# Kernel optimization log

Measured on AMD Instinct MI355X. Metric: run time of the kernel, lower is better.

## Reference

```python
import jax, jax.numpy as jnp
import numpy as np

K_INTERACT = 8  # k nearest context nodes per target hyperedge


def setup_inputs() -> dict:
    key = jax.random.key(0)
    ks = jax.random.split(key, 7)
    B, C, H, W = 4, 256, 64, 64
    s = 1.0 / np.sqrt(C).astype(np.float32)
    return {
        "X_target": jax.random.normal(ks[0], (B, C, H, W), jnp.float32),
        "X_context1": jax.random.normal(ks[1], (B, C, H, W), jnp.float32),
        "X_context2": jax.random.normal(ks[2], (B, C, H, W), jnp.float32),
        # HypergraphConv params: node2edge Linear (W1,b1), edge2node Linear (W2,b2)
        "W1": jax.random.normal(ks[3], (C, C), jnp.float32) * s,
        "b1": jax.random.normal(ks[4], (C,), jnp.float32) * s,
        "W2": jax.random.normal(ks[5], (C, C), jnp.float32) * s,
        "b2": jax.random.normal(ks[6], (C,), jnp.float32) * s,
    }


def _hypergraph_one(Xt, Xc, W1, b1, W2, b2, k):
    """Per-batch hypergraph message passing, sparse form of H^T X / H X.
    Xt: [N, C] target nodes, Xc: [Nc, C] context nodes.
    Edge j = {target j} U {k nearest context nodes of target j}.
    Equivalent to dense H_i [N+Nc, N] with degree normalization.
    """
    N, C = Xt.shape
    Nc = Xc.shape[0]
    # squared Euclidean cdist (same argmins as torch.cdist), knn = smallest-k
    d2 = (jnp.sum(Xt * Xt, axis=1)[:, None]
          + jnp.sum(Xc * Xc, axis=1)[None, :]
          - 2.0 * (Xt @ Xc.T))                      # [N, Nc]
    _, knn = jax.lax.top_k(-d2, k)                   # [N, k] context indices

    # node2edge linear transform on all nodes
    Xn_t = Xt @ W1 + b1                              # [N, C]
    Xn_c = Xc @ W1 + b1                              # [Nc, C]

    # X_edge = (H^T @ Xn) / deg_e ; deg_e = k+1 (self + k distinct knn)
    gathered = Xn_c[knn]                             # [N, k, C]
    X_edge = (Xn_t + gathered.sum(axis=1)) / jnp.float32(k + 1)

    # edge2node linear transform
    X_et = X_edge @ W2 + b2                          # [N, C]

    # X_node_new = (H @ X_et) / deg_v
    # target node v belongs only to edge v -> deg_v = 1
    out_t = X_et
    # context node c sums X_et[j] over edges j that selected it
    flat = knn.reshape(-1)                           # [N*k]
    contrib = jax.ops.segment_sum(
        jnp.broadcast_to(X_et[:, None, :], (N, k, C)).reshape(N * k, C),
        flat, num_segments=Nc)                       # [Nc, C]
    counts = jax.ops.segment_sum(jnp.ones((N * k,), jnp.float32),
                                 flat, num_segments=Nc)
    out_c = contrib / jnp.clip(counts, 1.0)[:, None]  # deg_v clamp_min(1)
    return out_t, out_c


def reference(X_target, X_context1, X_context2, W1, b1, W2, b2):
    B, C, H, W = X_target.shape
    N = H * W
    to_nodes = lambda x: x.transpose(0, 2, 3, 1).reshape(B, N, C)
    Xt = to_nodes(X_target)                                       # [B, N, C]
    Xc = jnp.concatenate([to_nodes(X_context1), to_nodes(X_context2)],
                         axis=1)                                  # [B, 2N, C]
    f = lambda xt, xc: _hypergraph_one(xt, xc, W1, b1, W2, b2, K_INTERACT)
    out_t, out_c = jax.vmap(f)(Xt, Xc)
    to_img = lambda x: x.reshape(B, H, W, C).transpose(0, 3, 1, 2)
    return (to_img(out_t), to_img(out_c[:, :N]), to_img(out_c[:, N:]))
```

## Files before the change

kernel.cpp:

```cpp
#include <hip/hip_runtime.h>
#include <math.h>
#include <float.h>

#define BATCH 4
#define CH    256
#define NT    4096
#define NCTX  8192
#define KI    8

#define CSEL    10
#define DNSPLIT 8
#define CTX_PER (NCTX / DNSPLIT)
#define NTILE   (CTX_PER / 32)
#define NKEY    (DNSPLIT * CSEL)
#define RESC    12

typedef __attribute__((ext_vector_type(8)))  __bf16 bf16x8;
typedef __attribute__((ext_vector_type(16))) float  f32x16;

__device__ __forceinline__ unsigned short bf16_rne(float v) {
  unsigned u = __float_as_uint(v);
  return (unsigned short)((u + 0x7fffu + ((u >> 16) & 1u)) >> 16);
}

__global__ __launch_bounds__(256) void k_transpose2(const float* __restrict__ Xt,
                                                    const float* __restrict__ Xc1,
                                                    const float* __restrict__ Xc2,
                                                    float* __restrict__ Q,
                                                    float* __restrict__ P,
                                                    unsigned short* __restrict__ XtBh,
                                                    unsigned short* __restrict__ XtBl,
                                                    unsigned short* __restrict__ XcBh,
                                                    unsigned short* __restrict__ XcBl,
                                                    float* __restrict__ nrm) {
  __shared__ float tile[64][33];
  __shared__ float ps[8][32];
  const int which = blockIdx.z >> 2, b = blockIdx.z & 3;
  const float* src;
  float* dF; unsigned short *dH, *dL; float* nrmp = nullptr;
  if (which == 0) {
    src = Xt + (long)b * CH * NT;
    dF = Q + (long)b * NT * CH;
    dH = XtBh + (long)b * NT * CH;  dL = XtBl + (long)b * NT * CH;
  } else if (which == 1) {
    src = Xc1 + (long)b * CH * NT;
    dF = P + (long)b * NCTX * CH;
    dH = XcBh + (long)b * NCTX * CH;  dL = XcBl + (long)b * NCTX * CH;
    nrmp = nrm + (long)b * NCTX;
  } else {
    src = Xc2 + (long)b * CH * NT;
    dF = P + ((long)b * NCTX + NT) * CH;
    dH = XcBh + ((long)b * NCTX + NT) * CH;  dL = XcBl + ((long)b * NCTX + NT) * CH;
    nrmp = nrm + (long)b * NCTX + NT;
  }
  const int m0 = blockIdx.x * 32, c0 = blockIdx.y * 64;
  const int tx = threadIdx.x, ty = threadIdx.y;
  float part = 0.f;
#pragma unroll
  for (int i = ty; i < 64; i += 8) {
    float v = src[(long)(c0 + i) * NT + (m0 + tx)];
    tile[i][tx] = v;
    part = fmaf(v, v, part);
  }
  if (which) ps[ty][tx] = part;
  __syncthreads();
#pragma unroll
  for (int i = ty; i < 32; i += 8) {
    float v0 = tile[2 * tx][i];
    float v1 = tile[2 * tx + 1][i];
    long o = (long)(m0 + i) * CH + (c0 + 2 * tx);
    float2 f2; f2.x = v0; f2.y = v1;
    *(float2*)&dF[o] = f2;
    unsigned short h0 = bf16_rne(v0), h1 = bf16_rne(v1);
    ushort2 h2; h2.x = h0; h2.y = h1;
    *(ushort2*)&dH[o] = h2;
    float hf0 = __uint_as_float((unsigned)h0 << 16);
    float hf1 = __uint_as_float((unsigned)h1 << 16);
    ushort2 l2; l2.x = bf16_rne(v0 - hf0); l2.y = bf16_rne(v1 - hf1);
    *(ushort2*)&dL[o] = l2;
  }
  if (which && ty == 0) {
    float s = 0.f;
#pragma unroll
    for (int j = 0; j < 8; ++j) s += ps[j][tx];
    atomicAdd(&nrmp[m0 + tx], -0.5f * s);
  }
}

__global__ __launch_bounds__(256) void k_wtrans(const float* __restrict__ W1,
                                                const float* __restrict__ W2,
                                                unsigned short* __restrict__ WT1h,
                                                unsigned short* __restrict__ WT1l,
                                                unsigned short* __restrict__ WT2h,
                                                unsigned short* __restrict__ WT2l) {
  __shared__ float tile[32][33];
  const float* W = blockIdx.z ? W2 : W1;
  unsigned short* WTh = blockIdx.z ? WT2h : WT1h;
  unsigned short* WTl = blockIdx.z ? WT2l : WT1l;
  const int n0 = blockIdx.x * 32, k0 = blockIdx.y * 32;
  const int tx = threadIdx.x, ty = threadIdx.y;
#pragma unroll
  for (int i = ty; i < 32; i += 8)
    tile[i][tx] = W[(k0 + i) * CH + (n0 + tx)];
  __syncthreads();
#pragma unroll
  for (int i = ty; i < 32; i += 8) {
    float v = tile[tx][i];
    int o = (n0 + i) * CH + (k0 + tx);
    unsigned short h = bf16_rne(v);
    WTh[o] = h;
    float hf = __uint_as_float((unsigned)h << 16);
    WTl[o] = bf16_rne(v - hf);
  }
}

__global__ __launch_bounds__(256) void k_dist_mfma(const __bf16* __restrict__ XcB,
                                                   const __bf16* __restrict__ XtB,
                                                   const float* __restrict__ nrm,
                                                   unsigned* __restrict__ cand) {
  __shared__ __bf16 lds[2][32 * CH];
  const int lid = blockIdx.x;
  const int xk = lid & 7;
  const int b = xk >> 1, jh = xk & 1;
  const int jw = (lid >> 3) & 15, split = lid >> 7;
  const int t = threadIdx.x, w = t >> 6, lane = t & 63;
  const int l31 = lane & 31, lh = lane >> 5;
  const int tgt0 = (jh * 16 + jw) * 128 + w * 32;
  const int cbase = split * CTX_PER;
  const float* nrmt = nrm + (long)b * NCTX + cbase;

  const __bf16* tp = XtB + ((long)b * NT + tgt0 + l31) * CH + lh * 8;
  bf16x8 bfrag[16];
#pragma unroll
  for (int s = 0; s < 16; ++s) bfrag[s] = *(const bf16x8*)(tp + s * 16);

  unsigned kd[CSEL];
#pragma unroll
  for (int q = 0; q < CSEL; ++q) kd[q] = 0xFFFFFFFFu;

  const __bf16* cp = XcB + ((long)b * NCTX + cbase + l31) * CH;

  auto STAGE = [&](int buf, int jt) {
#pragma unroll
    for (int r = 0; r < 4; ++r) {
      int c = r * 4 + w;
      const __bf16* src = cp + (long)jt * 32 * CH + (c * 2 + lh) * 8;
      __bf16* dst = &lds[buf][c * 512];
      __builtin_amdgcn_global_load_lds((const __attribute__((address_space(1))) void*)src,
                                       (__attribute__((address_space(3))) void*)dst,
                                       16, 0, 0);
    }
  };

  STAGE(0, 0);
  __syncthreads();

  int cur = 0;
  for (int jt = 0; jt < NTILE; ++jt) {
    if (jt + 1 < NTILE) STAGE(cur ^ 1, jt + 1);

    const int ct0 = jt * 32;
    f32x16 acc;
#pragma unroll
    for (int g = 0; g < 4; ++g) {
      float4 nv = *(const float4*)&nrmt[ct0 + 8 * g + 4 * lh];
      acc[4 * g + 0] = nv.x; acc[4 * g + 1] = nv.y;
      acc[4 * g + 2] = nv.z; acc[4 * g + 3] = nv.w;
    }
#pragma unroll
    for (int s = 0; s < 16; ++s) {
      bf16x8 a = *(const bf16x8*)(&lds[cur][s * 512 + lane * 8]);
      acc = __builtin_amdgcn_mfma_f32_32x32x16_bf16(a, bfrag[s], acc, 0, 0, 0);
    }

#pragma unroll
    for (int reg = 0; reg < 16; ++reg) {
      const int row = (reg & 3) + 8 * (reg >> 2) + lh * 4;
      float sc = fmaf(acc[reg], -2.0f, 512.0f);
      unsigned key = (__float_as_uint(sc) & 0xFFFFF800u) | (unsigned)ct0 | (unsigned)row;
#pragma unroll
      for (int q = 0; q < CSEL; ++q) {
        unsigned lo = min(key, kd[q]);
        key = max(key, kd[q]);
        kd[q] = lo;
      }
    }
    __syncthreads();
    cur ^= 1;
  }

  unsigned oth[CSEL];
#pragma unroll
  for (int q = 0; q < CSEL; ++q) oth[q] = (unsigned)__shfl_xor((int)kd[q], 32, 64);
  if (lh == 0) {
    long ob = (((long)b * NT + tgt0 + l31) * DNSPLIT + split) * CSEL;
#pragma unroll
    for (int q = 0; q < CSEL; ++q)
      cand[ob + q] = min(kd[q], oth[CSEL - 1 - q]);
  }
}

__global__ __launch_bounds__(64) void k_rescore(const float* __restrict__ XtT,
                                                const float* __restrict__ XcT,
                                                const unsigned* __restrict__ cand,
                                                int* __restrict__ knn,
                                                unsigned* __restrict__ counts) {
  const int n = blockIdx.x, b = blockIdx.y, lane = threadIdx.x;
  const int grp = lane >> 4, gl = lane & 15;
  __shared__ unsigned sk[NKEY];
  __shared__ int cidx[RESC];
  __shared__ double sd[RESC];
  __shared__ int sj[RESC];
  const unsigned* kp = cand + ((long)b * NT + n) * NKEY;
  unsigned k0 = kp[lane];
  unsigned k1 = (lane < NKEY - 64) ? kp[64 + lane] : 0xFFFFFFFFu;
  sk[lane] = k0;
  if (lane < NKEY - 64) sk[64 + lane] = k1;
  __syncthreads();
  int r0 = 0, r1 = 0;
  for (int i = 0; i < NKEY; ++i) {
    unsigned s = sk[i];
    r0 += (s < k0 || (s == k0 && i < lane)) ? 1 : 0;
    r1 += (s < k1 || (s == k1 && i < 64 + lane)) ? 1 : 0;
  }
  if (r0 < RESC) cidx[r0] = (lane / CSEL) * CTX_PER + (int)(k0 & 0x7FFu);
  if (lane < NKEY - 64 && r1 < RESC)
    cidx[r1] = ((64 + lane) / CSEL) * CTX_PER + (int)(k1 & 0x7FFu);
  __syncthreads();

  const float* xt = XtT + ((long)b * NT + n) * CH + gl * 16;
  double xa[16];
#pragma unroll
  for (int r = 0; r < 4; ++r) {
    float4 v = *(const float4*)(xt + r * 4);
    xa[4 * r + 0] = (double)v.x; xa[4 * r + 1] = (double)v.y;
    xa[4 * r + 2] = (double)v.z; xa[4 * r + 3] = (double)v.w;
  }
#pragma unroll
  for (int q0 = 0; q0 < RESC; q0 += 4) {
    int q = q0 + grp;
    int j = cidx[q];
    const float* xc = XcT + ((long)b * NCTX + j) * CH + gl * 16;
    double acc = 0.0;
#pragma unroll
    for (int r = 0; r < 4; ++r) {
      float4 v = *(const float4*)(xc + r * 4);
      double d0 = xa[4 * r + 0] - (double)v.x; acc = fma(d0, d0, acc);
      double d1 = xa[4 * r + 1] - (double)v.y; acc = fma(d1, d1, acc);
      double d2 = xa[4 * r + 2] - (double)v.z; acc = fma(d2, d2, acc);
      double d3 = xa[4 * r + 3] - (double)v.w; acc = fma(d3, d3, acc);
    }
#pragma unroll
    for (int off = 8; off > 0; off >>= 1) acc += __shfl_xor(acc, off, 64);
    if (gl == 0) { sd[q] = acc; sj[q] = j; }
  }
  __syncthreads();
  double dq = (lane < RESC) ? sd[lane] : DBL_MAX;
  int    jq = (lane < RESC) ? sj[lane] : 0x7fffffff;
  int rank = 0;
#pragma unroll
  for (int i = 0; i < RESC; ++i) {
    double di = sd[i]; int ji = sj[i];
    rank += (di < dq || (di == dq && ji < jq)) ? 1 : 0;
  }
  if (lane < RESC && rank < KI) {
    knn[((long)b * NT + n) * KI + rank] = jq;
    atomicAdd(&counts[(long)b * NCTX + jq], 1u);
  }
}

__global__ __launch_bounds__(256) void k_gemm_mfma(const unsigned short* __restrict__ Ah,
                                                   const unsigned short* __restrict__ Al,
                                                   const unsigned short* __restrict__ WTh,
                                                   const unsigned short* __restrict__ WTl,
                                                   const float* __restrict__ bias,
                                                   float* __restrict__ out, int M) {
  __shared__ __bf16 ldsH[32 * CH];
  __shared__ __bf16 ldsL[32 * CH];
  const int b = blockIdx.y;
  const int m0 = blockIdx.x * 32;
  const int t = threadIdx.x, w = t >> 6, lane = t & 63;
  const int l31 = lane & 31, lh = lane >> 5;
  const long abase = (long)b * M * CH;
  const unsigned short* pH = Ah + abase + (long)(m0 + l31) * CH;
  const unsigned short* pL = Al + abase + (long)(m0 + l31) * CH;
#pragma unroll
  for (int r = 0; r < 4; ++r) {
    int c = r * 4 + w;
    __builtin_amdgcn_global_load_lds(
        (const __attribute__((address_space(1))) void*)(pH + (c * 2 + lh) * 8),
        (__attribute__((address_space(3))) void*)&ldsH[c * 512], 16, 0, 0);
    __builtin_amdgcn_global_load_lds(
        (const __attribute__((address_space(1))) void*)(pL + (c * 2 + lh) * 8),
        (__attribute__((address_space(3))) void*)&ldsL[c * 512], 16, 0, 0);
  }
  __syncthreads();

  const int n0 = w * 64;
  f32x16 acc0, acc1;
#pragma unroll
  for (int i = 0; i < 16; ++i) { acc0[i] = 0.f; acc1[i] = 0.f; }
#pragma unroll
  for (int s = 0; s < 16; ++s) {
    bf16x8 ah = *(const bf16x8*)&ldsH[s * 512 + lane * 8];
    bf16x8 al = *(const bf16x8*)&ldsL[s * 512 + lane * 8];
    const int koff = lh * 8 + s * 16;
    bf16x8 bh0 = *(const bf16x8*)&WTh[(n0 + l31) * CH + koff];
    bf16x8 bl0 = *(const bf16x8*)&WTl[(n0 + l31) * CH + koff];
    bf16x8 bh1 = *(const bf16x8*)&WTh[(n0 + 32 + l31) * CH + koff];
    bf16x8 bl1 = *(const bf16x8*)&WTl[(n0 + 32 + l31) * CH + koff];
    acc0 = __builtin_amdgcn_mfma_f32_32x32x16_bf16(ah, bh0, acc0, 0, 0, 0);
    acc1 = __builtin_amdgcn_mfma_f32_32x32x16_bf16(ah, bh1, acc1, 0, 0, 0);
    acc0 = __builtin_amdgcn_mfma_f32_32x32x16_bf16(ah, bl0, acc0, 0, 0, 0);
    acc1 = __builtin_amdgcn_mfma_f32_32x32x16_bf16(ah, bl1, acc1, 0, 0, 0);
    acc0 = __builtin_amdgcn_mfma_f32_32x32x16_bf16(al, bh0, acc0, 0, 0, 0);
    acc1 = __builtin_amdgcn_mfma_f32_32x32x16_bf16(al, bh1, acc1, 0, 0, 0);
  }
  float* ob = out + abase;
  float bi0 = bias[n0 + l31], bi1 = bias[n0 + 32 + l31];
#pragma unroll
  for (int reg = 0; reg < 16; ++reg) {
    int row = (reg & 3) + 8 * (reg >> 2) + 4 * lh;
    ob[(long)(m0 + row) * CH + n0 + l31]      = acc0[reg] + bi0;
    ob[(long)(m0 + row) * CH + n0 + 32 + l31] = acc1[reg] + bi1;
  }
}

__global__ __launch_bounds__(256) void k_gather(const float* __restrict__ Xn_t,
                                                const float* __restrict__ Xn_c,
                                                const int* __restrict__ knn,
                                                unsigned short* __restrict__ XeH,
                                                unsigned short* __restrict__ XeL) {
  const int n = blockIdx.x, b = blockIdx.y, c = threadIdx.x;
  const int* kn = knn + ((long)b * NT + n) * KI;
  int j[KI];
#pragma unroll
  for (int q = 0; q < KI; ++q) j[q] = kn[q];
  float acc = Xn_t[((long)b * NT + n) * CH + c];
#pragma unroll
  for (int q = 0; q < KI; ++q) acc += Xn_c[((long)b * NCTX + j[q]) * CH + c];
  float xe = acc / 9.0f;
  long o = ((long)b * NT + n) * CH + c;
  unsigned short h = bf16_rne(xe);
  XeH[o] = h;
  float hf = __uint_as_float((unsigned)h << 16);
  XeL[o] = bf16_rne(xe - hf);
}

__global__ __launch_bounds__(256) void k_g2f(const unsigned short* __restrict__ XeH_g,
                                             const unsigned short* __restrict__ XeL_g,
                                             const unsigned short* __restrict__ WTh,
                                             const unsigned short* __restrict__ WTl,
                                             const float* __restrict__ bias,
                                             float* __restrict__ out_t,
                                             float* __restrict__ R) {
  __shared__ char smem[34816];
  __bf16* ldsH = (__bf16*)smem;
  __bf16* ldsL = (__bf16*)(smem + 16384);
  const int b = blockIdx.y;
  const int m0 = blockIdx.x * 32;
  const int t = threadIdx.x, w = t >> 6, lane = t & 63;
  const int l31 = lane & 31, lh = lane >> 5;
  const long abase = (long)b * NT * CH;
  const unsigned short* pH = XeH_g + abase + (long)(m0 + l31) * CH;
  const unsigned short* pL = XeL_g + abase + (long)(m0 + l31) * CH;
#pragma unroll
  for (int r = 0; r < 4; ++r) {
    int c = r * 4 + w;
    __builtin_amdgcn_global_load_lds(
        (const __attribute__((address_space(1))) void*)(pH + (c * 2 + lh) * 8),
        (__attribute__((address_space(3))) void*)&ldsH[c * 512], 16, 0, 0);
    __builtin_amdgcn_global_load_lds(
        (const __attribute__((address_space(1))) void*)(pL + (c * 2 + lh) * 8),
        (__attribute__((address_space(3))) void*)&ldsL[c * 512], 16, 0, 0);
  }
  __syncthreads();

  const unsigned short* wh0 = WTh + (long)(w * 64 + l31) * CH;
  const unsigned short* wl0 = WTl + (long)(w * 64 + l31) * CH;
  f32x16 acc0, acc1;
#pragma unroll
  for (int i = 0; i < 16; ++i) { acc0[i] = 0.f; acc1[i] = 0.f; }
#pragma unroll
  for (int s = 0; s < 16; ++s) {
    const int koff = lh * 8 + s * 16;
    bf16x8 beh = *(const bf16x8*)&ldsH[s * 512 + lane * 8];
    bf16x8 bel = *(const bf16x8*)&ldsL[s * 512 + lane * 8];
    bf16x8 ah0 = *(const bf16x8*)(const __bf16*)(wh0 + koff);
    bf16x8 al0 = *(const bf16x8*)(const __bf16*)(wl0 + koff);
    bf16x8 ah1 = *(const bf16x8*)(const __bf16*)(wh0 + 32 * CH + koff);
    bf16x8 al1 = *(const bf16x8*)(const __bf16*)(wl0 + 32 * CH + koff);
    acc0 = __builtin_amdgcn_mfma_f32_32x32x16_bf16(ah0, beh, acc0, 0, 0, 0);
    acc1 = __builtin_amdgcn_mfma_f32_32x32x16_bf16(ah1, beh, acc1, 0, 0, 0);
    acc0 = __builtin_amdgcn_mfma_f32_32x32x16_bf16(al0, beh, acc0, 0, 0, 0);
    acc1 = __builtin_amdgcn_mfma_f32_32x32x16_bf16(al1, beh, acc1, 0, 0, 0);
    acc0 = __builtin_amdgcn_mfma_f32_32x32x16_bf16(ah0, bel, acc0, 0, 0, 0);
    acc1 = __builtin_amdgcn_mfma_f32_32x32x16_bf16(ah1, bel, acc1, 0, 0, 0);
  }
  __syncthreads();

  float* S = (float*)smem;
  float* ot = out_t + (long)b * CH * NT + m0;
#pragma unroll
  for (int reg = 0; reg < 16; ++reg) {
    const int row = (reg & 3) + 8 * (reg >> 2) + 4 * lh;
    const int ch0 = w * 64 + row, ch1 = ch0 + 32;
    float v0 = acc0[reg] + bias[ch0];
    float v1 = acc1[reg] + bias[ch1];
    S[ch0 * 33 + l31] = v0;
    S[ch1 * 33 + l31] = v1;
    ot[(long)ch0 * NT + l31] = v0;
    ot[(long)ch1 * NT + l31] = v1;
  }
  __syncthreads();
  const int n = t & 31, cg = t >> 5;
  float* rrow = R + ((long)b * NT + m0 + n) * CH;
#pragma unroll
  for (int kk = 0; kk < 8; ++kk) {
    const int c = cg * 32 + kk * 4;
    float4 v;
    v.x = S[(c + 0) * 33 + n];
    v.y = S[(c + 1) * 33 + n];
    v.z = S[(c + 2) * 33 + n];
    v.w = S[(c + 3) * 33 + n];
    *(float4*)(rrow + c) = v;
  }
}

__global__ __launch_bounds__(256) void k_scatter(const float* __restrict__ Xet,
                                                 const int* __restrict__ knn,
                                                 float* __restrict__ contrib) {
  const int n = blockIdx.x, b = blockIdx.y, c = threadIdx.x;
  const float v = Xet[((long)b * NT + n) * CH + c];
  const int* kn = knn + ((long)b * NT + n) * KI;
#pragma unroll
  for (int q = 0; q < KI; ++q)
    atomicAdd(&contrib[((long)b * NCTX + kn[q]) * CH + c], v);
}

__global__ __launch_bounds__(256) void k_fin_c(const float* __restrict__ contrib,
                                               const unsigned* __restrict__ counts,
                                               float* __restrict__ out1,
                                               float* __restrict__ out2) {
  __shared__ float tile[32][33];
  const int b = blockIdx.z;
  const int j0 = blockIdx.x * 32, c0 = blockIdx.y * 32;
  const int tx = threadIdx.x, ty = threadIdx.y;
#pragma unroll
  for (int i = ty; i < 32; i += 8) {
    float cnt = fmaxf((float)counts[(long)b * NCTX + j0 + i], 1.0f);
    tile[i][tx] = contrib[((long)b * NCTX + j0 + i) * CH + c0 + tx] / cnt;
  }
  __syncthreads();
  float* outp = (j0 < NT) ? (out1 + (long)b * CH * NT + j0)
                          : (out2 + (long)b * CH * NT + (j0 - NT));
#pragma unroll
  for (int i = ty; i < 32; i += 8)
    outp[(long)(c0 + i) * NT + tx] = tile[tx][i];
}

extern "C" void kernel_launch(void* const* d_in, const int* in_sizes, int n_in,
                              void* d_out, int out_size, void* d_ws, size_t ws_size,
                              hipStream_t stream) {
  const float* Xt  = (const float*)d_in[0];
  const float* Xc1 = (const float*)d_in[1];
  const float* Xc2 = (const float*)d_in[2];
  const float* W1  = (const float*)d_in[3];
  const float* b1  = (const float*)d_in[4];
  const float* W2  = (const float*)d_in[5];
  const float* b2  = (const float*)d_in[6];
  float* out = (float*)d_out;

  float* P = (float*)d_ws;
  float* Q = P + (long)BATCH * NCTX * CH;
  float* R = Q + (long)BATCH * NT * CH;
  float* nrm = R + (long)BATCH * NT * CH;
  unsigned* counts = (unsigned*)(nrm + (long)BATCH * NCTX);
  int* knn = (int*)(counts + (long)BATCH * NCTX);
  unsigned short* WT1h = (unsigned short*)(knn + (long)BATCH * NT * KI);
  unsigned short* WT1l = WT1h + CH * CH;
  unsigned short* WT2h = WT1l + CH * CH;
  unsigned short* WT2l = WT2h + CH * CH;

  unsigned* cand = (unsigned*)R;

  unsigned short* XcBh = (unsigned short*)d_out;
  unsigned short* XtBh = XcBh + (long)BATCH * NCTX * CH;
  unsigned short* XcBl = XtBh + (long)BATCH * NT * CH;
  unsigned short* XtBl = XcBl + (long)BATCH * NCTX * CH;

  float* Xn_c = P;
  float* Xn_t = R;
  unsigned short* XeH = (unsigned short*)Q;
  unsigned short* XeL = XeH + (long)BATCH * NT * CH;

  float* out_t  = out;
  float* out_c1 = out + (long)BATCH * CH * NT;
  float* out_c2 = out + 2L * BATCH * CH * NT;

  dim3 tb(32, 8);

  hipMemsetAsync(nrm, 0, (size_t)BATCH * NCTX * 8, stream);

  k_wtrans<<<dim3(8, 8, 2), tb, 0, stream>>>(W1, W2, WT1h, WT1l, WT2h, WT2l);

  k_transpose2<<<dim3(NT / 32, CH / 64, 12), tb, 0, stream>>>(
      Xt, Xc1, Xc2, Q, P, XtBh, XtBl, XcBh, XcBl, nrm);

  k_dist_mfma<<<dim3(8 * 16 * DNSPLIT), 256, 0, stream>>>(
      (const __bf16*)XcBh, (const __bf16*)XtBh, nrm, cand);

  k_rescore<<<dim3(NT, BATCH), 64, 0, stream>>>(Q, P, cand, knn, counts);

  k_gemm_mfma<<<dim3(NT / 32, BATCH), 256, 0, stream>>>(XtBh, XtBl, WT1h, WT1l, b1, Xn_t, NT);
  k_gemm_mfma<<<dim3(NCTX / 32, BATCH), 256, 0, stream>>>(XcBh, XcBl, WT1h, WT1l, b1, Xn_c, NCTX);

  k_gather<<<dim3(NT, BATCH), 256, 0, stream>>>(Xn_t, Xn_c, knn, XeH, XeL);

  hipMemsetAsync(P, 0, (size_t)BATCH * NCTX * CH * 4, stream);

  k_g2f<<<dim3(NT / 32, BATCH), 256, 0, stream>>>(XeH, XeL, WT2h, WT2l, b2, out_t, R);

  k_scatter<<<dim3(NT, BATCH), 256, 0, stream>>>(R, knn, P);
  k_fin_c<<<dim3(NCTX / 32, CH / 32, BATCH), tb, 0, stream>>>(P, counts, out_c1, out_c2);
}
```

Measured before the change: 437.1 us.

## Merge distance kNN and node2edge GEMMs into one launch; fuse prep kernels

The weight transpose is merged into the input transpose/split kernel, which also widens its tiles to 128 channels and writes float4/ushort4 vectors. When the workspace is large enough, the distance top-k kernel and both node2edge GEMMs run as one grid, using separate buffers for candidates and Xn_c so the two can run concurrently. Otherwise the old sequence is kept. The finalize kernel uses 128-row tiles with float4 stores and a reciprocal multiply in place of a divide. This cuts launch count and lets GEMM blocks fill idle CUs during the distance pass, at the cost of extra workspace and a branchy fused kernel whose register/LDS footprint is set by the larger path.

```diff
diff --git a/kernel.cpp b/kernel.cpp
--- a/kernel.cpp
+++ b/kernel.cpp
@@ -23,180 +23,305 @@
   return (unsigned short)((u + 0x7fffu + ((u >> 16) & 1u)) >> 16);
 }
 
-__global__ __launch_bounds__(256) void k_transpose2(const float* __restrict__ Xt,
-                                                    const float* __restrict__ Xc1,
-                                                    const float* __restrict__ Xc2,
-                                                    float* __restrict__ Q,
-                                                    float* __restrict__ P,
-                                                    unsigned short* __restrict__ XtBh,
-                                                    unsigned short* __restrict__ XtBl,
-                                                    unsigned short* __restrict__ XcBh,
-                                                    unsigned short* __restrict__ XcBl,
-                                                    float* __restrict__ nrm) {
-  __shared__ float tile[64][33];
+__global__ __launch_bounds__(256) void k_prep(const float* __restrict__ Xt,
+                                              const float* __restrict__ Xc1,
+                                              const float* __restrict__ Xc2,
+                                              float* __restrict__ Q,
+                                              float* __restrict__ P,
+                                              unsigned short* __restrict__ XtBh,
+                                              unsigned short* __restrict__ XtBl,
+                                              unsigned short* __restrict__ XcBh,
+                                              unsigned short* __restrict__ XcBl,
+                                              float* __restrict__ nrm,
+                                              const float* __restrict__ W1,
+                                              const float* __restrict__ W2,
+                                              unsigned short* __restrict__ WT1h,
+                                              unsigned short* __restrict__ WT1l,
+                                              unsigned short* __restrict__ WT2h,
+                                              unsigned short* __restrict__ WT2l) {
+  __shared__ float tile[128][33];
   __shared__ float ps[8][32];
-  const int which = blockIdx.z >> 2, b = blockIdx.z & 3;
-  const float* src;
-  float* dF; unsigned short *dH, *dL; float* nrmp = nullptr;
-  if (which == 0) {
-    src = Xt + (long)b * CH * NT;
-    dF = Q + (long)b * NT * CH;
-    dH = XtBh + (long)b * NT * CH;  dL = XtBl + (long)b * NT * CH;
-  } else if (which == 1) {
-    src = Xc1 + (long)b * CH * NT;
-    dF = P + (long)b * NCTX * CH;
-    dH = XcBh + (long)b * NCTX * CH;  dL = XcBl + (long)b * NCTX * CH;
-    nrmp = nrm + (long)b * NCTX;
+  const int bid = blockIdx.x;
+  const int tx = threadIdx.x, ty = threadIdx.y;
+
+  if (bid < 3072) {
+    const int x = bid & 127, y = (bid >> 7) & 1, z = bid >> 8;
+    const int which = z >> 2, b = z & 3;
+    const float* src;
+    float* dF; unsigned short *dH, *dL; float* nrmp = nullptr;
+    if (which == 0) {
+      src = Xt + (long)b * CH * NT;
+      dF = Q + (long)b * NT * CH;
+      dH = XtBh + (long)b * NT * CH;  dL = XtBl + (long)b * NT * CH;
+    } else if (which == 1) {
+      src = Xc1 + (long)b * CH * NT;
+      dF = P + (long)b * NCTX * CH;
+      dH = XcBh + (long)b * NCTX * CH;  dL = XcBl + (long)b * NCTX * CH;
+      nrmp = nrm + (long)b * NCTX;
+    } else {
+      src = Xc2 + (long)b * CH * NT;
+      dF = P + ((long)b * NCTX + NT) * CH;
+      dH = XcBh + ((long)b * NCTX + NT) * CH;  dL = XcBl + ((long)b * NCTX + NT) * CH;
+      nrmp = nrm + (long)b * NCTX + NT;
+    }
+    const int m0 = x * 32, c0 = y * 128;
+    float part = 0.f;
+#pragma unroll
+    for (int i = ty; i < 128; i += 8) {
+      float v = src[(long)(c0 + i) * NT + (m0 + tx)];
+      tile[i][tx] = v;
+      part = fmaf(v, v, part);
+    }
+    if (which) ps[ty][tx] = part;
+    __syncthreads();
+#pragma unroll
+    for (int i = ty; i < 32; i += 8) {
+      float v0 = tile[4 * tx + 0][i];
+      float v1 = tile[4 * tx + 1][i];
+      float v2 = tile[4 * tx + 2][i];
+      float v3 = tile[4 * tx + 3][i];
+      long o = (long)(m0 + i) * CH + (c0 + 4 * tx);
+      float4 f4; f4.x = v0; f4.y = v1; f4.z = v2; f4.w = v3;
+      *(float4*)&dF[o] = f4;
+      unsigned short h0 = bf16_rne(v0), h1 = bf16_rne(v1), h2 = bf16_rne(v2), h3 = bf16_rne(v3);
+      ushort4 h4; h4.x = h0; h4.y = h1; h4.z = h2; h4.w = h3;
+      *(ushort4*)&dH[o] = h4;
+      ushort4 l4;
+      l4.x = bf16_rne(v0 - __uint_as_float((unsigned)h0 << 16));
+      l4.y = bf16_rne(v1 - __uint_as_float((unsigned)h1 << 16));
+      l4.z = bf16_rne(v2 - __uint_as_float((unsigned)h2 << 16));
+      l4.w = bf16_rne(v3 - __uint_as_float((unsigned)h3 << 16));
+      *(ushort4*)&dL[o] = l4;
+    }
+    if (which && ty == 0) {
+      float s = 0.f;
+#pragma unroll
+      for (int j = 0; j < 8; ++j) s += ps[j][tx];
+      atomicAdd(&nrmp[m0 + tx], -0.5f * s);
+    }
   } else {
-    src = Xc2 + (long)b * CH * NT;
-    dF = P + ((long)b * NCTX + NT) * CH;
-    dH = XcBh + ((long)b * NCTX + NT) * CH;  dL = XcBl + ((long)b * NCTX + NT) * CH;
-    nrmp = nrm + (long)b * NCTX + NT;
-  }
-  const int m0 = blockIdx.x * 32, c0 = blockIdx.y * 64;
-  const int tx = threadIdx.x, ty = threadIdx.y;
-  float part = 0.f;
-#pragma unroll
-  for (int i = ty; i < 64; i += 8) {
-    float v = src[(long)(c0 + i) * NT + (m0 + tx)];
-    tile[i][tx] = v;
-    part = fmaf(v, v, part);
-  }
-  if (which) ps[ty][tx] = part;
-  __syncthreads();
-#pragma unroll
-  for (int i = ty; i < 32; i += 8) {
-    float v0 = tile[2 * tx][i];
-    float v1 = tile[2 * tx + 1][i];
-    long o = (long)(m0 + i) * CH + (c0 + 2 * tx);
-    float2 f2; f2.x = v0; f2.y = v1;
-    *(float2*)&dF[o] = f2;
-    unsigned short h0 = bf16_rne(v0), h1 = bf16_rne(v1);
-    ushort2 h2; h2.x = h0; h2.y = h1;
-    *(ushort2*)&dH[o] = h2;
-    float hf0 = __uint_as_float((unsigned)h0 << 16);
-    float hf1 = __uint_as_float((unsigned)h1 << 16);
-    ushort2 l2; l2.x = bf16_rne(v0 - hf0); l2.y = bf16_rne(v1 - hf1);
-    *(ushort2*)&dL[o] = l2;
-  }
-  if (which && ty == 0) {
-    float s = 0.f;
-#pragma unroll
-    for (int j = 0; j < 8; ++j) s += ps[j][tx];
-    atomicAdd(&nrmp[m0 + tx], -0.5f * s);
-  }
-}
-
-__global__ __launch_bounds__(256) void k_wtrans(const float* __restrict__ W1,
-                                                const float* __restrict__ W2,
-                                                unsigned short* __restrict__ WT1h,
-                                                unsigned short* __restrict__ WT1l,
-                                                unsigned short* __restrict__ WT2h,
-                                                unsigned short* __restrict__ WT2l) {
-  __shared__ float tile[32][33];
-  const float* W = blockIdx.z ? W2 : W1;
-  unsigned short* WTh = blockIdx.z ? WT2h : WT1h;
-  unsigned short* WTl = blockIdx.z ? WT2l : WT1l;
-  const int n0 = blockIdx.x * 32, k0 = blockIdx.y * 32;
-  const int tx = threadIdx.x, ty = threadIdx.y;
-#pragma unroll
-  for (int i = ty; i < 32; i += 8)
-    tile[i][tx] = W[(k0 + i) * CH + (n0 + tx)];
-  __syncthreads();
-#pragma unroll
-  for (int i = ty; i < 32; i += 8) {
-    float v = tile[tx][i];
-    int o = (n0 + i) * CH + (k0 + tx);
-    unsigned short h = bf16_rne(v);
-    WTh[o] = h;
-    float hf = __uint_as_float((unsigned)h << 16);
-    WTl[o] = bf16_rne(v - hf);
-  }
-}
-
-__global__ __launch_bounds__(256) void k_dist_mfma(const __bf16* __restrict__ XcB,
-                                                   const __bf16* __restrict__ XtB,
-                                                   const float* __restrict__ nrm,
-                                                   unsigned* __restrict__ cand) {
+    const int r = bid - 3072;
+    const int n0 = (r & 7) * 32, k0 = ((r >> 3) & 7) * 32;
+    const float* W = (r >> 6) ? W2 : W1;
+    unsigned short* WTh = (r >> 6) ? WT2h : WT1h;
+    unsigned short* WTl = (r >> 6) ? WT2l : WT1l;
+#pragma unroll
+    for (int i = ty; i < 32; i += 8)
+      tile[i][tx] = W[(k0 + i) * CH + (n0 + tx)];
+    __syncthreads();
+#pragma unroll
+    for (int i = ty; i < 32; i += 8) {
+      float v = tile[tx][i];
+      int o = (n0 + i) * CH + (k0 + tx);
+      unsigned short h = bf16_rne(v);
+      WTh[o] = h;
+      WTl[o] = bf16_rne(v - __uint_as_float((unsigned)h << 16));
+    }
+  }
+}
+
+__global__ __launch_bounds__(256) void k_main(const __bf16* __restrict__ XcB,
+                                              const __bf16* __restrict__ XtB,
+                                              const float* __restrict__ nrm,
+                                              unsigned* __restrict__ cand,
+                                              const unsigned short* __restrict__ XtBh,
+                                              const unsigned short* __restrict__ XtBl,
+                                              const unsigned short* __restrict__ XcBh,
+                                              const unsigned short* __restrict__ XcBl,
+                                              const unsigned short* __restrict__ WTh,
+                                              const unsigned short* __restrict__ WTl,
+                                              const float* __restrict__ bias,
+                                              float* __restrict__ outT,
+                                              float* __restrict__ outC) {
   __shared__ __bf16 lds[2][32 * CH];
-  const int lid = blockIdx.x;
-  const int xk = lid & 7;
-  const int b = xk >> 1, jh = xk & 1;
-  const int jw = (lid >> 3) & 15, split = lid >> 7;
+  const int bid = blockIdx.x;
   const int t = threadIdx.x, w = t >> 6, lane = t & 63;
   const int l31 = lane & 31, lh = lane >> 5;
-  const int tgt0 = (jh * 16 + jw) * 128 + w * 32;
-  const int cbase = split * CTX_PER;
-  const float* nrmt = nrm + (long)b * NCTX + cbase;
-
-  const __bf16* tp = XtB + ((long)b * NT + tgt0 + l31) * CH + lh * 8;
-  bf16x8 bfrag[16];
-#pragma unroll
-  for (int s = 0; s < 16; ++s) bfrag[s] = *(const bf16x8*)(tp + s * 16);
-
-  unsigned kd[CSEL];
-#pragma unroll
-  for (int q = 0; q < CSEL; ++q) kd[q] = 0xFFFFFFFFu;
-
-  const __bf16* cp = XcB + ((long)b * NCTX + cbase + l31) * CH;
-
-  auto STAGE = [&](int buf, int jt) {
+
+  if (bid < 1024) {
+    const int xk = bid & 7;
+    const int b = xk >> 1, jh = xk & 1;
+    const int jw = (bid >> 3) & 15, split = bid >> 7;
+    const int tgt0 = (jh * 16 + jw) * 128 + w * 32;
+    const int cbase = split * CTX_PER;
+    const float* nrmt = nrm + (long)b * NCTX + cbase;
+
+    const __bf16* tp = XtB + ((long)b * NT + tgt0 + l31) * CH + lh * 8;
+    bf16x8 bfrag[16];
+#pragma unroll
+    for (int s = 0; s < 16; ++s) bfrag[s] = *(const bf16x8*)(tp + s * 16);
+
+    unsigned kd[CSEL];
+#pragma unroll
+    for (int q = 0; q < CSEL; ++q) kd[q] = 0xFFFFFFFFu;
+
+    const __bf16* cp = XcB + ((long)b * NCTX + cbase + l31) * CH;
+
+    auto STAGE = [&](int buf, int jt) {
+#pragma unroll
+      for (int r = 0; r < 4; ++r) {
+        int c = r * 4 + w;
+        const __bf16* src = cp + (long)jt * 32 * CH + (c * 2 + lh) * 8;
+        __bf16* dst = &lds[buf][c * 512];
+        __builtin_amdgcn_global_load_lds((const __attribute__((address_space(1))) void*)src,
+                                         (__attribute__((address_space(3))) void*)dst,
+                                         16, 0, 0);
+      }
+    };
+
+    STAGE(0, 0);
+    __syncthreads();
+
+    int cur = 0;
+    for (int jt = 0; jt < NTILE; ++jt) {
+      if (jt + 1 < NTILE) STAGE(cur ^ 1, jt + 1);
+
+      const int ct0 = jt * 32;
+      f32x16 acc;
+#pragma unroll
+      for (int g = 0; g < 4; ++g) {
+        float4 nv = *(const float4*)&nrmt[ct0 + 8 * g + 4 * lh];
+        acc[4 * g + 0] = nv.x; acc[4 * g + 1] = nv.y;
+        acc[4 * g + 2] = nv.z; acc[4 * g + 3] = nv.w;
+      }
+#pragma unroll
+      for (int s = 0; s < 16; ++s) {
+        bf16x8 a = *(const bf16x8*)(&lds[cur][s * 512 + lane * 8]);
+        acc = __builtin_amdgcn_mfma_f32_32x32x16_bf16(a, bfrag[s], acc, 0, 0, 0);
+      }
+
+#pragma unroll
+      for (int reg = 0; reg < 16; ++reg) {
+        const int row = (reg & 3) + 8 * (reg >> 2) + lh * 4;
+        float sc = fmaf(acc[reg], -2.0f, 512.0f);
+        unsigned key = (__float_as_uint(sc) & 0xFFFFF800u) | (unsigned)ct0 | (unsigned)row;
+#pragma unroll
+        for (int q = 0; q < CSEL; ++q) {
+          unsigned lo = min(key, kd[q]);
+          key = max(key, kd[q]);
+          kd[q] = lo;
+        }
+      }
+      __syncthreads();
+      cur ^= 1;
+    }
+
+    unsigned oth[CSEL];
+#pragma unroll
+    for (int q = 0; q < CSEL; ++q) oth[q] = (unsigned)__shfl_xor((int)kd[q], 32, 64);
+    if (lh == 0) {
+      long ob = (((long)b * NT + tgt0 + l31) * DNSPLIT + split) * CSEL;
+#pragma unroll
+      for (int q = 0; q < CSEL; ++q)
+        cand[ob + q] = min(kd[q], oth[CSEL - 1 - q]);
+    }
+  } else {
+    int g = bid - 1024;
+    const unsigned short *Ah, *Al; float* out; int M, m0, b;
+    if (g < 512) { Ah = XtBh; Al = XtBl; out = outT; M = NT;   m0 = (g & 127) * 32; b = g >> 7; }
+    else { g -= 512; Ah = XcBh; Al = XcBl; out = outC; M = NCTX; m0 = (g & 255) * 32; b = g >> 8; }
+    __bf16* ldsH = lds[0];
+    __bf16* ldsL = lds[1];
+    const long abase = (long)b * M * CH;
+    const unsigned short* pH = Ah + abase + (long)(m0 + l31) * CH;
+    const unsigned short* pL = Al + abase + (long)(m0 + l31) * CH;
 #pragma unroll
     for (int r = 0; r < 4; ++r) {
       int c = r * 4 + w;
-      const __bf16* src = cp + (long)jt * 32 * CH + (c * 2 + lh) * 8;
-      __bf16* dst = &lds[buf][c * 512];
-      __builtin_amdgcn_global_load_lds((const __attribute__((address_space(1))) void*)src,
-                                       (__attribute__((address_space(3))) void*)dst,
-                                       16, 0, 0);
-    }
-  };
-
-  STAGE(0, 0);
-  __syncthreads();
-
-  int cur = 0;
-  for (int jt = 0; jt < NTILE; ++jt) {
-    if (jt + 1 < NTILE) STAGE(cur ^ 1, jt + 1);
-
-    const int ct0 = jt * 32;
-    f32x16 acc;
-#pragma unroll
-    for (int g = 0; g < 4; ++g) {
-      float4 nv = *(const float4*)&nrmt[ct0 + 8 * g + 4 * lh];
-      acc[4 * g + 0] = nv.x; acc[4 * g + 1] = nv.y;
-      acc[4 * g + 2] = nv.z; acc[4 * g + 3] = nv.w;
-    }
+      __builtin_amdgcn_global_load_lds(
+          (const __attribute__((address_space(1))) void*)(pH + (c * 2 + lh) * 8),
+          (__attribute__((address_space(3))) void*)&ldsH[c * 512], 16, 0, 0);
+      __builtin_amdgcn_global_load_lds(
+          (const __attribute__((address_space(1))) void*)(pL + (c * 2 + lh) * 8),
+          (__attribute__((address_space(3))) void*)&ldsL[c * 512], 16, 0, 0);
+    }
+    __syncthreads();
+
+    const int n0 = w * 64;
+    f32x16 acc0, acc1;
+#pragma unroll
+    for (int i = 0; i < 16; ++i) { acc0[i] = 0.f; acc1[i] = 0.f; }
 #pragma unroll
     for (int s = 0; s < 16; ++s) {
-      bf16x8 a = *(const bf16x8*)(&lds[cur][s * 512 + lane * 8]);
-      acc = __builtin_amdgcn_mfma_f32_32x32x16_bf16(a, bfrag[s], acc, 0, 0, 0);
-    }
-
+      bf16x8 ah = *(const bf16x8*)&ldsH[s * 512 + lane * 8];
+      bf16x8 al = *(const bf16x8*)&ldsL[s * 512 + lane * 8];
+      const int koff = lh * 8 + s * 16;
+      bf16x8 bh0 = *(const bf16x8*)&WTh[(n0 + l31) * CH + koff];
+      bf16x8 bl0 = *(const bf16x8*)&WTl[(n0 + l31) * CH + koff];
+      bf16x8 bh1 = *(const bf16x8*)&WTh[(n0 + 32 + l31) * CH + koff];
+      bf16x8 bl1 = *(const bf16x8*)&WTl[(n0 + 32 + l31) * CH + koff];
+      acc0 = __builtin_amdgcn_mfma_f32_32x32x16_bf16(ah, bh0, acc0, 0, 0, 0);
+      acc1 = __builtin_amdgcn_mfma_f32_32x32x16_bf16(ah, bh1, acc1, 0, 0, 0);
+      acc0 = __builtin_amdgcn_mfma_f32_32x32x16_bf16(ah, bl0, acc0, 0, 0, 0);
+      acc1 = __builtin_amdgcn_mfma_f32_32x32x16_bf16(ah, bl1, acc1, 0, 0, 0);
+      acc0 = __builtin_amdgcn_mfma_f32_32x32x16_bf16(al, bh0, acc0, 0, 0, 0);
+      acc1 = __builtin_amdgcn_mfma_f32_32x32x16_bf16(al, bh1, acc1, 0, 0, 0);
+    }
+    float* ob = out + abase;
+    float bi0 = bias[n0 + l31], bi1 = bias[n0 + 32 + l31];
 #pragma unroll
     for (int reg = 0; reg < 16; ++reg) {
-      const int row = (reg & 3) + 8 * (reg >> 2) + lh * 4;
-      float sc = fmaf(acc[reg], -2.0f, 512.0f);
-      unsigned key = (__float_as_uint(sc) & 0xFFFFF800u) | (unsigned)ct0 | (unsigned)row;
-#pragma unroll
-      for (int q = 0; q < CSEL; ++q) {
-        unsigned lo = min(key, kd[q]);
-        key = max(key, kd[q]);
-        kd[q] = lo;
-      }
-    }
-    __syncthreads();
-    cur ^= 1;
-  }
-
-  unsigned oth[CSEL];
-#pragma unroll
-  for (int q = 0; q < CSEL; ++q) oth[q] = (unsigned)__shfl_xor((int)kd[q], 32, 64);
-  if (lh == 0) {
-    long ob = (((long)b * NT + tgt0 + l31) * DNSPLIT + split) * CSEL;
-#pragma unroll
-    for (int q = 0; q < CSEL; ++q)
-      cand[ob + q] = min(kd[q], oth[CSEL - 1 - q]);
+      int row = (reg & 3) + 8 * (reg >> 2) + 4 * lh;
+      ob[(long)(m0 + row) * CH + n0 + l31]      = acc0[reg] + bi0;
+      ob[(long)(m0 + row) * CH + n0 + 32 + l31] = acc1[reg] + bi1;
+    }
+  }
+}
+
+__global__ __launch_bounds__(256) void k_gemm_mfma(const unsigned short* __restrict__ Ah,
+                                                   const unsigned short* __restrict__ Al,
+                                                   const unsigned short* __restrict__ WTh,
+                                                   const unsigned short* __restrict__ WTl,
+                                                   const float* __restrict__ bias,
+                                                   float* __restrict__ out, int M) {
+  __shared__ __bf16 ldsH[32 * CH];
+  __shared__ __bf16 ldsL[32 * CH];
+  const int b = blockIdx.y;
+  const int m0 = blockIdx.x * 32;
+  const int t = threadIdx.x, w = t >> 6, lane = t & 63;
+  const int l31 = lane & 31, lh = lane >> 5;
+  const long abase = (long)b * M * CH;
+  const unsigned short* pH = Ah + abase + (long)(m0 + l31) * CH;
+  const unsigned short* pL = Al + abase + (long)(m0 + l31) * CH;
+#pragma unroll
+  for (int r = 0; r < 4; ++r) {
+    int c = r * 4 + w;
+    __builtin_amdgcn_global_load_lds(
+        (const __attribute__((address_space(1))) void*)(pH + (c * 2 + lh) * 8),
+        (__attribute__((address_space(3))) void*)&ldsH[c * 512], 16, 0, 0);
+    __builtin_amdgcn_global_load_lds(
+        (const __attribute__((address_space(1))) void*)(pL + (c * 2 + lh) * 8),
+        (__attribute__((address_space(3))) void*)&ldsL[c * 512], 16, 0, 0);
+  }
+  __syncthreads();
+
+  const int n0 = w * 64;
+  f32x16 acc0, acc1;
+#pragma unroll
+  for (int i = 0; i < 16; ++i) { acc0[i] = 0.f; acc1[i] = 0.f; }
+#pragma unroll
+  for (int s = 0; s < 16; ++s) {
+    bf16x8 ah = *(const bf16x8*)&ldsH[s * 512 + lane * 8];
+    bf16x8 al = *(const bf16x8*)&ldsL[s * 512 + lane * 8];
+    const int koff = lh * 8 + s * 16;
+    bf16x8 bh0 = *(const bf16x8*)&WTh[(n0 + l31) * CH + koff];
+    bf16x8 bl0 = *(const bf16x8*)&WTl[(n0 + l31) * CH + koff];
+    bf16x8 bh1 = *(const bf16x8*)&WTh[(n0 + 32 + l31) * CH + koff];
+    bf16x8 bl1 = *(const bf16x8*)&WTl[(n0 + 32 + l31) * CH + koff];
+    acc0 = __builtin_amdgcn_mfma_f32_32x32x16_bf16(ah, bh0, acc0, 0, 0, 0);
+    acc1 = __builtin_amdgcn_mfma_f32_32x32x16_bf16(ah, bh1, acc1, 0, 0, 0);
+    acc0 = __builtin_amdgcn_mfma_f32_32x32x16_bf16(ah, bl0, acc0, 0, 0, 0);
+    acc1 = __builtin_amdgcn_mfma_f32_32x32x16_bf16(ah, bl1, acc1, 0, 0, 0);
+    acc0 = __builtin_amdgcn_mfma_f32_32x32x16_bf16(al, bh0, acc0, 0, 0, 0);
+    acc1 = __builtin_amdgcn_mfma_f32_32x32x16_bf16(al, bh1, acc1, 0, 0, 0);
+  }
+  float* ob = out + abase;
+  float bi0 = bias[n0 + l31], bi1 = bias[n0 + 32 + l31];
+#pragma unroll
+  for (int reg = 0; reg < 16; ++reg) {
+    int row = (reg & 3) + 8 * (reg >> 2) + 4 * lh;
+    ob[(long)(m0 + row) * CH + n0 + l31]      = acc0[reg] + bi0;
+    ob[(long)(m0 + row) * CH + n0 + 32 + l31] = acc1[reg] + bi1;
   }
 }
 
@@ -269,63 +394,6 @@
   }
 }
 
-__global__ __launch_bounds__(256) void k_gemm_mfma(const unsigned short* __restrict__ Ah,
-                                                   const unsigned short* __restrict__ Al,
-                                                   const unsigned short* __restrict__ WTh,
-                                                   const unsigned short* __restrict__ WTl,
-                                                   const float* __restrict__ bias,
-                                                   float* __restrict__ out, int M) {
-  __shared__ __bf16 ldsH[32 * CH];
-  __shared__ __bf16 ldsL[32 * CH];
-  const int b = blockIdx.y;
-  const int m0 = blockIdx.x * 32;
-  const int t = threadIdx.x, w = t >> 6, lane = t & 63;
-  const int l31 = lane & 31, lh = lane >> 5;
-  const long abase = (long)b * M * CH;
-  const unsigned short* pH = Ah + abase + (long)(m0 + l31) * CH;
-  const unsigned short* pL = Al + abase + (long)(m0 + l31) * CH;
-#pragma unroll
-  for (int r = 0; r < 4; ++r) {
-    int c = r * 4 + w;
-    __builtin_amdgcn_global_load_lds(
-        (const __attribute__((address_space(1))) void*)(pH + (c * 2 + lh) * 8),
-        (__attribute__((address_space(3))) void*)&ldsH[c * 512], 16, 0, 0);
-    __builtin_amdgcn_global_load_lds(
-        (const __attribute__((address_space(1))) void*)(pL + (c * 2 + lh) * 8),
-        (__attribute__((address_space(3))) void*)&ldsL[c * 512], 16, 0, 0);
-  }
-  __syncthreads();
-
-  const int n0 = w * 64;
-  f32x16 acc0, acc1;
-#pragma unroll
-  for (int i = 0; i < 16; ++i) { acc0[i] = 0.f; acc1[i] = 0.f; }
-#pragma unroll
-  for (int s = 0; s < 16; ++s) {
-    bf16x8 ah = *(const bf16x8*)&ldsH[s * 512 + lane * 8];
-    bf16x8 al = *(const bf16x8*)&ldsL[s * 512 + lane * 8];
-    const int koff = lh * 8 + s * 16;
-    bf16x8 bh0 = *(const bf16x8*)&WTh[(n0 + l31) * CH + koff];
-    bf16x8 bl0 = *(const bf16x8*)&WTl[(n0 + l31) * CH + koff];
-    bf16x8 bh1 = *(const bf16x8*)&WTh[(n0 + 32 + l31) * CH + koff];
-    bf16x8 bl1 = *(const bf16x8*)&WTl[(n0 + 32 + l31) * CH + koff];
-    acc0 = __builtin_amdgcn_mfma_f32_32x32x16_bf16(ah, bh0, acc0, 0, 0, 0);
-    acc1 = __builtin_amdgcn_mfma_f32_32x32x16_bf16(ah, bh1, acc1, 0, 0, 0);
-    acc0 = __builtin_amdgcn_mfma_f32_32x32x16_bf16(ah, bl0, acc0, 0, 0, 0);
-    acc1 = __builtin_amdgcn_mfma_f32_32x32x16_bf16(ah, bl1, acc1, 0, 0, 0);
-    acc0 = __builtin_amdgcn_mfma_f32_32x32x16_bf16(al, bh0, acc0, 0, 0, 0);
-    acc1 = __builtin_amdgcn_mfma_f32_32x32x16_bf16(al, bh1, acc1, 0, 0, 0);
-  }
-  float* ob = out + abase;
-  float bi0 = bias[n0 + l31], bi1 = bias[n0 + 32 + l31];
-#pragma unroll
-  for (int reg = 0; reg < 16; ++reg) {
-    int row = (reg & 3) + 8 * (reg >> 2) + 4 * lh;
-    ob[(long)(m0 + row) * CH + n0 + l31]      = acc0[reg] + bi0;
-    ob[(long)(m0 + row) * CH + n0 + 32 + l31] = acc1[reg] + bi1;
-  }
-}
-
 __global__ __launch_bounds__(256) void k_gather(const float* __restrict__ Xn_t,
                                                 const float* __restrict__ Xn_c,
                                                 const int* __restrict__ knn,
@@ -343,8 +411,7 @@
   long o = ((long)b * NT + n) * CH + c;
   unsigned short h = bf16_rne(xe);
   XeH[o] = h;
-  float hf = __uint_as_float((unsigned)h << 16);
-  XeL[o] = bf16_rne(xe - hf);
+  XeL[o] = bf16_rne(xe - __uint_as_float((unsigned)h << 16));
 }
 
 __global__ __launch_bounds__(256) void k_g2f(const unsigned short* __restrict__ XeH_g,
@@ -442,21 +509,27 @@
                                                const unsigned* __restrict__ counts,
                                                float* __restrict__ out1,
                                                float* __restrict__ out2) {
-  __shared__ float tile[32][33];
+  __shared__ float tile[128][33];
   const int b = blockIdx.z;
-  const int j0 = blockIdx.x * 32, c0 = blockIdx.y * 32;
+  const int j0 = blockIdx.x * 128, c0 = blockIdx.y * 32;
   const int tx = threadIdx.x, ty = threadIdx.y;
 #pragma unroll
-  for (int i = ty; i < 32; i += 8) {
+  for (int i = ty; i < 128; i += 8) {
     float cnt = fmaxf((float)counts[(long)b * NCTX + j0 + i], 1.0f);
-    tile[i][tx] = contrib[((long)b * NCTX + j0 + i) * CH + c0 + tx] / cnt;
+    tile[i][tx] = contrib[((long)b * NCTX + j0 + i) * CH + c0 + tx] * (1.0f / cnt);
   }
   __syncthreads();
   float* outp = (j0 < NT) ? (out1 + (long)b * CH * NT + j0)
                           : (out2 + (long)b * CH * NT + (j0 - NT));
 #pragma unroll
-  for (int i = ty; i < 32; i += 8)
-    outp[(long)(c0 + i) * NT + tx] = tile[tx][i];
+  for (int i = ty; i < 32; i += 8) {
+    float4 v;
+    v.x = tile[4 * tx + 0][i];
+    v.y = tile[4 * tx + 1][i];
+    v.z = tile[4 * tx + 2][i];
+    v.w = tile[4 * tx + 3][i];
+    *(float4*)&outp[(long)(c0 + i) * NT + 4 * tx] = v;
+  }
 }
 
 extern "C" void kernel_launch(void* const* d_in, const int* in_sizes, int n_in,
@@ -481,16 +554,20 @@
   unsigned short* WT1l = WT1h + CH * CH;
   unsigned short* WT2h = WT1l + CH * CH;
   unsigned short* WT2l = WT2h + CH * CH;
-
-  unsigned* cand = (unsigned*)R;
+  float* Xn_c_fat = (float*)(WT2l + CH * CH);
+  unsigned* cand_fat = (unsigned*)(Xn_c_fat + (long)BATCH * NCTX * CH);
+  const size_t need_fat = (size_t)((char*)(cand_fat + (long)BATCH * NT * NKEY) - (char*)d_ws);
+  const bool fat = ws_size >= need_fat;
+
+  unsigned* cand = fat ? cand_fat : (unsigned*)R;
+  float* Xn_c = fat ? Xn_c_fat : P;
+  float* Xn_t = R;
 
   unsigned short* XcBh = (unsigned short*)d_out;
   unsigned short* XtBh = XcBh + (long)BATCH * NCTX * CH;
   unsigned short* XcBl = XtBh + (long)BATCH * NT * CH;
   unsigned short* XtBl = XcBl + (long)BATCH * NCTX * CH;
 
-  float* Xn_c = P;
-  float* Xn_t = R;
   unsigned short* XeH = (unsigned short*)Q;
   unsigned short* XeL = XeH + (long)BATCH * NT * CH;
 
@@ -502,18 +579,22 @@
 
   hipMemsetAsync(nrm, 0, (size_t)BATCH * NCTX * 8, stream);
 
-  k_wtrans<<<dim3(8, 8, 2), tb, 0, stream>>>(W1, W2, WT1h, WT1l, WT2h, WT2l);
-
-  k_transpose2<<<dim3(NT / 32, CH / 64, 12), tb, 0, stream>>>(
-      Xt, Xc1, Xc2, Q, P, XtBh, XtBl, XcBh, XcBl, nrm);
-
-  k_dist_mfma<<<dim3(8 * 16 * DNSPLIT), 256, 0, stream>>>(
-      (const __bf16*)XcBh, (const __bf16*)XtBh, nrm, cand);
-
-  k_rescore<<<dim3(NT, BATCH), 64, 0, stream>>>(Q, P, cand, knn, counts);
-
-  k_gemm_mfma<<<dim3(NT / 32, BATCH), 256, 0, stream>>>(XtBh, XtBl, WT1h, WT1l, b1, Xn_t, NT);
-  k_gemm_mfma<<<dim3(NCTX / 32, BATCH), 256, 0, stream>>>(XcBh, XcBl, WT1h, WT1l, b1, Xn_c, NCTX);
+  k_prep<<<dim3(3072 + 128), tb, 0, stream>>>(Xt, Xc1, Xc2, Q, P, XtBh, XtBl, XcBh, XcBl, nrm,
+                                              W1, W2, WT1h, WT1l, WT2h, WT2l);
+
+  if (fat) {
+    k_main<<<dim3(1024 + 512 + 1024), 256, 0, stream>>>(
+        (const __bf16*)XcBh, (const __bf16*)XtBh, nrm, cand,
+        XtBh, XtBl, XcBh, XcBl, WT1h, WT1l, b1, Xn_t, Xn_c);
+    k_rescore<<<dim3(NT, BATCH), 64, 0, stream>>>(Q, P, cand, knn, counts);
+  } else {
+    k_main<<<dim3(1024), 256, 0, stream>>>(
+        (const __bf16*)XcBh, (const __bf16*)XtBh, nrm, cand,
+        XtBh, XtBl, XcBh, XcBl, WT1h, WT1l, b1, Xn_t, Xn_c);
+    k_rescore<<<dim3(NT, BATCH), 64, 0, stream>>>(Q, P, cand, knn, counts);
+    k_gemm_mfma<<<dim3(NT / 32, BATCH), 256, 0, stream>>>(XtBh, XtBl, WT1h, WT1l, b1, Xn_t, NT);
+    k_gemm_mfma<<<dim3(NCTX / 32, BATCH), 256, 0, stream>>>(XcBh, XcBl, WT1h, WT1l, b1, Xn_c, NCTX);
+  }
 
   k_gather<<<dim3(NT, BATCH), 256, 0, stream>>>(Xn_t, Xn_c, knn, XeH, XeL);
 
@@ -522,5 +603,5 @@
   k_g2f<<<dim3(NT / 32, BATCH), 256, 0, stream>>>(XeH, XeL, WT2h, WT2l, b2, out_t, R);
 
   k_scatter<<<dim3(NT, BATCH), 256, 0, stream>>>(R, knn, P);
-  k_fin_c<<<dim3(NCTX / 32, CH / 32, BATCH), tb, 0, stream>>>(P, counts, out_c1, out_c2);
-}
+  k_fin_c<<<dim3(NCTX / 128, CH / 32, BATCH), tb, 0, stream>>>(P, counts, out_c1, out_c2);
+}
```

Result: faster. 399.8 us (-8.5%).
